# Kernel optimization log

Hardware: AMD Instinct MI355X
Metric: run time of the kernel (lower is better)

Reference implementation:

```python
import jax, jax.numpy as jnp
import numpy as np

N_NODES = 100000
N_EDGES = 1600000
N_GRAPHS = 256
D_IN = 128
D_HID = 128
D_OUT = 64


def graph_conv(x, src, dst, W_rel, b_rel, W_root):
    # PyG GraphConv: out = lin_rel(mean_{j->i} x_j) + lin_root(x)
    msgs = jax.ops.segment_sum(x[src], dst, num_segments=N_NODES)  # [N, d]
    deg = jax.ops.segment_sum(jnp.ones((src.shape[0],), x.dtype), dst, num_segments=N_NODES)
    agg = msgs / jnp.maximum(deg, 1.0)[:, None]
    return agg @ W_rel + b_rel + x @ W_root


def setup_inputs() -> dict:
    key = jax.random.key(0)
    ks = jax.random.split(key, 12)
    x = jax.random.normal(ks[0], (N_NODES, D_IN), dtype=jnp.float32)
    edge_index = jax.random.randint(ks[1], (2, N_EDGES), 0, N_NODES, dtype=jnp.int64)
    batch = jnp.sort(jax.random.randint(ks[2], (N_NODES,), 0, N_GRAPHS, dtype=jnp.int64))
    def lin(k, fan_in, fan_out):
        bound = 1.0 / np.sqrt(fan_in)
        return jax.random.uniform(k, (fan_in, fan_out), jnp.float32, -bound, bound)
    inp = {
        "x": x, "edge_index": edge_index, "batch": batch,
        "W1_rel": lin(ks[3], D_IN, D_HID), "b1_rel": jnp.zeros((D_HID,), jnp.float32), "W1_root": lin(ks[4], D_IN, D_HID),
        "W2_rel": lin(ks[5], D_HID, D_HID), "b2_rel": jnp.zeros((D_HID,), jnp.float32), "W2_root": lin(ks[6], D_HID, D_HID),
        "W3_rel": lin(ks[7], D_HID, D_HID), "b3_rel": jnp.zeros((D_HID,), jnp.float32), "W3_root": lin(ks[8], D_HID, D_HID),
        "Wl": lin(ks[9], D_HID, D_OUT), "bl": jnp.zeros((D_OUT,), jnp.float32),
    }
    return inp


def reference(x, edge_index, batch, W1_rel, b1_rel, W1_root, W2_rel, b2_rel, W2_root,
              W3_rel, b3_rel, W3_root, Wl, bl):
    src, dst = edge_index[0], edge_index[1]
    h = jax.nn.relu(graph_conv(x, src, dst, W1_rel, b1_rel, W1_root))
    h = jax.nn.relu(graph_conv(h, src, dst, W2_rel, b2_rel, W2_root))
    h = graph_conv(h, src, dst, W3_rel, b3_rel, W3_root)
    # global mean pool over graphs
    sums = jax.ops.segment_sum(h, batch, num_segments=N_GRAPHS)          # [G, d]
    cnts = jax.ops.segment_sum(jnp.ones((h.shape[0],), h.dtype), batch, num_segments=N_GRAPHS)
    pooled = sums / jnp.maximum(cnts, 1.0)[:, None]
    # dropout is identity at inference
    return pooled @ Wl + bl  # [G, D_OUT]
```

## Files before the change

### kernel.cpp

```cpp
#include <hip/hip_runtime.h>
#include <hip/hip_bf16.h>

#define N_NODES  100000
#define N_EDGES  1600000
#define N_GRAPHS 256
#define DCH      128
#define DOUT     64
#define NB       391
#define PADB     512
#define SLACK    4608
#define CHUNK    2048
#define PCH      32

typedef short v8s __attribute__((ext_vector_type(8)));
typedef float v4f __attribute__((ext_vector_type(4)));

static __device__ __forceinline__ float bf2f(unsigned short u) {
    unsigned int x = ((unsigned int)u) << 16;
    return __builtin_bit_cast(float, x);
}
static __device__ __forceinline__ unsigned short f2bf(float f) {
    unsigned int x = __builtin_bit_cast(unsigned int, f);
    unsigned int r = (x + 0x7fffu + ((x >> 16) & 1u)) >> 16;
    return (unsigned short)r;
}
static __device__ __forceinline__ int clampi(int v, int lo, int hi) {
    return v < lo ? lo : (v > hi ? hi : v);
}

__global__ void cvt_kernel(const float* __restrict__ in, unsigned short* __restrict__ out) {
    size_t i = ((size_t)blockIdx.x * blockDim.x + threadIdx.x) * 4;
    if (i + 3 < (size_t)N_NODES * DCH) {
        float4 f = *reinterpret_cast<const float4*>(in + i);
        uint2 o;
        o.x = ((unsigned)f2bf(f.y) << 16) | (unsigned)f2bf(f.x);
        o.y = ((unsigned)f2bf(f.w) << 16) | (unsigned)f2bf(f.z);
        *reinterpret_cast<uint2*>(out + i) = o;
    }
}

__global__ void __launch_bounds__(256) binA_kernel(const int* __restrict__ src, const int* __restrict__ dst,
                                                   int* __restrict__ gcur, uint2* __restrict__ region) {
    __shared__ uint2 stage[CHUNK];
    __shared__ int hcnt[PADB], hcnt2[PADB], hoff[PADB], garr[PADB];
    __shared__ int s2[256];
    int tid = threadIdx.x;
    int e0  = blockIdx.x * CHUNK;
    int nedge = N_EDGES - e0; if (nedge > CHUNK) nedge = CHUNK;

    for (int b = tid; b < PADB; b += 256) { hcnt[b] = 0; hcnt2[b] = 0; }
    __syncthreads();

    int es[CHUNK / 256], ed[CHUNK / 256];
    #pragma unroll
    for (int j = 0; j < CHUNK / 256; j++) {
        int e = e0 + j * 256 + tid;
        if (e < N_EDGES) {
            es[j] = clampi(src[e], 0, N_NODES - 1);
            ed[j] = clampi(dst[e], 0, N_NODES - 1);
            atomicAdd(&hcnt[ed[j] >> 8], 1);
        } else { es[j] = -1; ed[j] = 0; }
    }
    __syncthreads();

    int v0 = hcnt[2 * tid], v1 = hcnt[2 * tid + 1];
    s2[tid] = v0 + v1; __syncthreads();
    for (int off = 1; off < 256; off <<= 1) {
        int x = (tid >= off) ? s2[tid - off] : 0;
        __syncthreads();
        s2[tid] += x;
        __syncthreads();
    }
    int excl = s2[tid] - (v0 + v1);
    hoff[2 * tid] = excl; hoff[2 * tid + 1] = excl + v0;
    __syncthreads();

    for (int b = tid; b < NB; b += 256) {
        int c = hcnt[b];
        garr[b] = b * SLACK + ((c > 0) ? atomicAdd(&gcur[b], c) : 0);
    }
    __syncthreads();

    #pragma unroll
    for (int j = 0; j < CHUNK / 256; j++) {
        if (es[j] >= 0) {
            int b = ed[j] >> 8;
            int pos = atomicAdd(&hcnt2[b], 1) + hoff[b];
            stage[pos] = (uint2){(unsigned)es[j], (unsigned)ed[j]};
        }
    }
    __syncthreads();

    for (int i = tid; i < nedge; i += 256) {
        uint2 en = stage[i];
        int b = (int)(en.y >> 8);
        int gpos = garr[b] + (i - hoff[b]);
        if (gpos < (b + 1) * SLACK) region[gpos] = en;
    }
}

__global__ void __launch_bounds__(256) scan_kernel(const int* __restrict__ gcur,
                                                   int* __restrict__ hoffG, int* __restrict__ rowptr) {
    __shared__ int s2[256];
    int tid = threadIdx.x;
    int c0 = gcur[2 * tid];     if (c0 > SLACK) c0 = SLACK;
    int c1 = gcur[2 * tid + 1]; if (c1 > SLACK) c1 = SLACK;
    s2[tid] = c0 + c1; __syncthreads();
    for (int off = 1; off < 256; off <<= 1) {
        int x = (tid >= off) ? s2[tid - off] : 0;
        __syncthreads();
        s2[tid] += x;
        __syncthreads();
    }
    int excl = s2[tid] - (c0 + c1);
    hoffG[2 * tid] = excl; hoffG[2 * tid + 1] = excl + c0;
    if (tid == 255) rowptr[N_NODES] = s2[255];
}

__global__ void __launch_bounds__(256) binFinish_kernel(const uint2* __restrict__ region, const int* __restrict__ gcur,
                                                        const int* __restrict__ hoffG,
                                                        int* __restrict__ rowptr, int* __restrict__ csr) {
    __shared__ int h[256], sc[256], cur[256];
    int b = blockIdx.x, tid = threadIdx.x;
    h[tid] = 0;
    int base = hoffG[b];
    int size = gcur[b]; if (size > SLACK) size = SLACK;
    int node0 = b * 256;
    __syncthreads();
    for (int j = tid; j < size; j += 256) {
        unsigned loc = region[b * SLACK + j].y - (unsigned)node0;
        if (loc < 256u) atomicAdd(&h[loc], 1);
    }
    __syncthreads();
    int v = h[tid]; sc[tid] = v; __syncthreads();
    for (int off = 1; off < 256; off <<= 1) {
        int x = (tid >= off) ? sc[tid - off] : 0;
        __syncthreads();
        sc[tid] += x;
        __syncthreads();
    }
    int myptr = base + sc[tid] - v;
    int node = node0 + tid;
    if (node < N_NODES) rowptr[node] = myptr;
    cur[tid] = myptr;
    __syncthreads();
    for (int j = tid; j < size; j += 256) {
        uint2 en = region[b * SLACK + j];
        unsigned loc = en.y - (unsigned)node0;
        if (loc < 256u) {
            int p = atomicAdd(&cur[loc], 1);
            if (p >= 0 && p < N_EDGES) csr[p] = (int)en.x;
        }
    }
}

__global__ void wfrag_kernel(const float* __restrict__ W1rel, const float* __restrict__ W1root,
                             const float* __restrict__ W2rel, const float* __restrict__ W2root,
                             const float* __restrict__ W3rel, const float* __restrict__ W3root,
                             unsigned short* __restrict__ frag) {
    int gid = blockIdx.x * blockDim.x + threadIdx.x;
    if (gid >= 3 * 8 * 8 * 64) return;
    int lane = gid & 63;
    int nt   = (gid >> 6) & 7;
    int kt   = (gid >> 9) & 7;
    int L    = gid >> 12;
    const float* rel  = (L == 0) ? W1rel  : (L == 1) ? W2rel  : W3rel;
    const float* root = (L == 0) ? W1root : (L == 1) ? W2root : W3root;
    int n  = nt * 16 + (lane & 15);
    int k0 = kt * 32 + (lane >> 4) * 8;
    unsigned short o[8];
    #pragma unroll
    for (int j = 0; j < 8; j++) {
        int k = k0 + j;
        float w = (k < 128) ? rel[k * 128 + n] : root[(k - 128) * 128 + n];
        o[j] = f2bf(w);
    }
    uint4 u;
    u.x = (unsigned)o[0] | ((unsigned)o[1] << 16);
    u.y = (unsigned)o[2] | ((unsigned)o[3] << 16);
    u.z = (unsigned)o[4] | ((unsigned)o[5] << 16);
    u.w = (unsigned)o[6] | ((unsigned)o[7] << 16);
    *reinterpret_cast<uint4*>(frag + (size_t)gid * 8) = u;
}

__global__ void __launch_bounds__(128, 4) layer_kernel(
    const unsigned short* __restrict__ hin,
    const int* __restrict__ rowptr, const int* __restrict__ csr,
    const unsigned short* __restrict__ frag, const float* __restrict__ bias,
    unsigned short* __restrict__ hout, int relu)
{
    __shared__ __attribute__((aligned(16))) unsigned short As[2][32 * DCH];
    const int wave = threadIdx.x >> 6;
    const int lane = threadIdx.x & 63;
    const int l16  = lane & 15;
    const int quad = lane >> 4;
    const int base = blockIdx.x * 64 + wave * 32;
    if (base >= N_NODES) return;

    char* Asb = reinterpret_cast<char*>(As[wave]);

    int rp = rowptr[base + (lane < 33 ? lane : 32)];
    const int R0 = __builtin_amdgcn_readlane(rp, 0);
    const int R1 = __builtin_amdgcn_readlane(rp, 32);

    int ni     = 0;
    int nstart = R0;
    int nend   = __builtin_amdgcn_readlane(rp, 1);
    float a0 = 0.f, a1 = 0.f;

    int t0  = csr[R0 + l16];
    int idx = (R0 + l16 < R1) ? t0 : N_NODES;

    for (int e0 = R0; e0 < R1; e0 += 16) {
        int en   = e0 + 16 + l16;
        int tn   = csr[en];
        int idxn = (en < R1) ? tn : N_NODES;

        unsigned v[16];
        #pragma unroll
        for (int j = 0; j < 16; j++) {
            int s = __builtin_amdgcn_readlane(idx, j);
            v[j] = *reinterpret_cast<const unsigned*>(hin + (size_t)s * DCH + lane * 2);
        }

        #pragma unroll
        for (int j = 0; j < 16; j++) {
            int e = e0 + j;
            while (ni < 32 && e == nend) {
                int deg = nend - nstart;
                float inv = 1.0f / (float)(deg > 1 ? deg : 1);
                unsigned o = ((unsigned)f2bf(a1 * inv) << 16) | (unsigned)f2bf(a0 * inv);
                *reinterpret_cast<unsigned*>(Asb + ni * 256 + ((lane * 4) ^ ((ni & 7) << 4))) = o;
                a0 = 0.f; a1 = 0.f;
                ni++;
                nstart = nend;
                nend = __builtin_amdgcn_readlane(rp, ni + 1);
            }
            a0 += bf2f((unsigned short)(v[j] & 0xffffu));
            a1 += bf2f((unsigned short)(v[j] >> 16));
        }
        idx = idxn;
    }
    while (ni < 32) {
        int deg = nend - nstart;
        float inv = 1.0f / (float)(deg > 1 ? deg : 1);
        unsigned o = ((unsigned)f2bf(a1 * inv) << 16) | (unsigned)f2bf(a0 * inv);
        *reinterpret_cast<unsigned*>(Asb + ni * 256 + ((lane * 4) ^ ((ni & 7) << 4))) = o;
        a0 = 0.f; a1 = 0.f;
        ni++;
        nstart = nend;
        nend = __builtin_amdgcn_readlane(rp, ni + 1 < 33 ? ni + 1 : 32);
    }

    v4f acc[2][8];
    #pragma unroll
    for (int h = 0; h < 2; h++)
        #pragma unroll
        for (int nt = 0; nt < 8; nt++) acc[h][nt] = (v4f){0.f, 0.f, 0.f, 0.f};

    #pragma unroll
    for (int kt = 0; kt < 8; kt++) {
        v8s a0v, a1v;
        if (kt < 4) {
            int co = (kt * 64 + quad * 16) ^ ((l16 & 7) << 4);
            a0v = *reinterpret_cast<const v8s*>(Asb + l16 * 256 + co);
            a1v = *reinterpret_cast<const v8s*>(Asb + (16 + l16) * 256 + co);
        } else {
            int ak = (kt - 4) * 32 + quad * 8;
            a0v = *reinterpret_cast<const v8s*>(hin + (size_t)(base + l16) * DCH + ak);
            a1v = *reinterpret_cast<const v8s*>(hin + (size_t)(base + 16 + l16) * DCH + ak);
        }
        #pragma unroll
        for (int nt = 0; nt < 8; nt++) {
            v8s b = *reinterpret_cast<const v8s*>(frag + (((size_t)(kt * 8 + nt)) * 64 + lane) * 8);
            acc[0][nt] = __builtin_amdgcn_mfma_f32_16x16x32_bf16(a0v, b, acc[0][nt], 0, 0, 0);
            acc[1][nt] = __builtin_amdgcn_mfma_f32_16x16x32_bf16(a1v, b, acc[1][nt], 0, 0, 0);
        }
    }
    #pragma unroll
    for (int h = 0; h < 2; h++) {
        int mbase = base + h * 16 + quad * 4;
        #pragma unroll
        for (int nt = 0; nt < 8; nt++) {
            int n = nt * 16 + l16;
            float bv = bias[n];
            #pragma unroll
            for (int r = 0; r < 4; r++) {
                float v = acc[h][nt][r] + bv;
                if (relu) v = fmaxf(v, 0.f);
                hout[(size_t)(mbase + r) * DCH + n] = f2bf(v);
            }
        }
    }
}

__global__ void __launch_bounds__(128) pool_kernel(const unsigned short* __restrict__ h,
                                                   const int* __restrict__ batch,
                                                   float* __restrict__ psum) {
    int c  = threadIdx.x;
    int n0 = blockIdx.x * PCH;
    int n1 = n0 + PCH < N_NODES ? n0 + PCH : N_NODES;
    if (n0 >= n1) return;
    int cur = clampi(batch[n0], 0, N_GRAPHS - 1);
    float acc = 0.f;
    for (int n = n0; n < n1; n++) {
        int g = clampi(batch[n], 0, N_GRAPHS - 1);
        if (g != cur) {
            atomicAdd(&psum[cur * DCH + c], acc);
            acc = 0.f; cur = g;
        }
        acc += bf2f(h[(size_t)n * DCH + c]);
    }
    atomicAdd(&psum[cur * DCH + c], acc);
}

static __device__ __forceinline__ int lowerb(const int* __restrict__ a, int n, int key) {
    int lo = 0, hi = n;
    while (lo < hi) { int mid = (lo + hi) >> 1; if (a[mid] < key) lo = mid + 1; else hi = mid; }
    return lo;
}

__global__ void __launch_bounds__(64) final_kernel(const float* __restrict__ psum,
                                                   const int* __restrict__ batch,
                                                   const float* __restrict__ Wl, const float* __restrict__ bl,
                                                   float* __restrict__ out) {
    __shared__ float ps[DCH];
    __shared__ int bounds[2];
    int g = blockIdx.x, tid = threadIdx.x;
    if (tid == 0) {
        bounds[0] = lowerb(batch, N_NODES, g);
        bounds[1] = lowerb(batch, N_NODES, g + 1);
    }
    __syncthreads();
    int cnt = bounds[1] - bounds[0];
    float inv = 1.0f / (float)(cnt > 1 ? cnt : 1);
    ps[tid] = psum[g * DCH + tid] * inv;
    ps[tid + 64] = psum[g * DCH + tid + 64] * inv;
    __syncthreads();
    float o = 0.f;
    #pragma unroll 4
    for (int c = 0; c < DCH; c++) o += ps[c] * Wl[c * DOUT + tid];
    out[g * DOUT + tid] = o + bl[tid];
}

extern "C" void kernel_launch(void* const* d_in, const int* in_sizes, int n_in,
                              void* d_out, int out_size, void* d_ws, size_t ws_size,
                              hipStream_t stream) {
    const float* x     = (const float*)d_in[0];
    const int*   edge  = (const int*)d_in[1];
    const int*   src   = edge;
    const int*   dst   = edge + N_EDGES;
    const int*   batch = (const int*)d_in[2];
    const float* W1rel  = (const float*)d_in[3];
    const float* b1     = (const float*)d_in[4];
    const float* W1root = (const float*)d_in[5];
    const float* W2rel  = (const float*)d_in[6];
    const float* b2     = (const float*)d_in[7];
    const float* W2root = (const float*)d_in[8];
    const float* W3rel  = (const float*)d_in[9];
    const float* b3     = (const float*)d_in[10];
    const float* W3root = (const float*)d_in[11];
    const float* Wl     = (const float*)d_in[12];
    const float* bl     = (const float*)d_in[13];
    float* out = (float*)d_out;

    char* ws = (char*)d_ws;
    size_t off = 0;
    auto carve = [&](size_t bytes) -> void* {
        void* p = ws + off;
        off += (bytes + 255) & ~(size_t)255;
        return p;
    };
    int*            rowptr  = (int*)carve((size_t)(N_NODES + 1) * 4);
    int*            csr     = (int*)carve((size_t)(N_EDGES + 64) * 4);
    int*            gcur    = (int*)carve((size_t)PADB * 4 + (size_t)N_GRAPHS * DCH * 4);
    float*          psum    = (float*)(gcur + PADB);
    int*            hoffG   = (int*)carve((size_t)PADB * 4);
    unsigned short* frag    = (unsigned short*)carve((size_t)3 * 8 * 8 * 64 * 8 * 2);
    unsigned short* B1      = (unsigned short*)carve((size_t)(N_NODES + 1) * DCH * 2);
    unsigned short* B2      = (unsigned short*)carve((size_t)(N_NODES + 1) * DCH * 2);
    uint2*          region  = (uint2*)B1;

    hipMemsetAsync(gcur, 0, (size_t)PADB * 4 + (size_t)N_GRAPHS * DCH * 4, stream);
    hipMemsetAsync(B1 + (size_t)N_NODES * DCH, 0, (size_t)DCH * 2, stream);
    hipMemsetAsync(B2 + (size_t)N_NODES * DCH, 0, (size_t)DCH * 2, stream);

    binA_kernel<<<(N_EDGES + CHUNK - 1) / CHUNK, 256, 0, stream>>>(src, dst, gcur, region);
    scan_kernel<<<1, 256, 0, stream>>>(gcur, hoffG, rowptr);
    binFinish_kernel<<<NB, 256, 0, stream>>>(region, gcur, hoffG, rowptr, csr);
    cvt_kernel<<<(N_NODES * DCH / 4 + 255) / 256, 256, 0, stream>>>(x, B2);
    wfrag_kernel<<<(3 * 8 * 8 * 64 + 255) / 256, 256, 0, stream>>>(W1rel, W1root, W2rel, W2root, W3rel, W3root, frag);

    const int layerGrid = (N_NODES + 63) / 64;

    layer_kernel<<<layerGrid, 128, 0, stream>>>(B2, rowptr, csr, frag,         b1, B1, 1);
    layer_kernel<<<layerGrid, 128, 0, stream>>>(B1, rowptr, csr, frag + 32768, b2, B2, 1);
    layer_kernel<<<layerGrid, 128, 0, stream>>>(B2, rowptr, csr, frag + 65536, b3, B1, 0);

    pool_kernel<<<(N_NODES + PCH - 1) / PCH, 128, 0, stream>>>(B1, batch, psum);
    final_kernel<<<N_GRAPHS, 64, 0, stream>>>(psum, batch, Wl, bl, out);
}
```

Before: 414.9 us.

## Fuse mean-pool into last layer, merge prep kernels, use 16-row waves

The third GraphConv layer now accumulates its bias-added outputs straight into the per-graph pool sums with atomics, which removes the separate pool kernel and the write and re-read of the final hidden features. Input conversion, weight fragment packing and zeroing of the padding rows are merged into one prep kernel, replacing two launches and two memsets. The layer kernel now gives each wave 16 nodes instead of 32, with 256-thread blocks. This spreads the gather work over more waves for better latency hiding, at the cost of reusing each weight fragment across half as many rows.

```diff
diff --git a/kernel.cpp b/kernel.cpp
--- a/kernel.cpp
+++ b/kernel.cpp
@@ -10,7 +10,6 @@
 #define PADB     512
 #define SLACK    4608
 #define CHUNK    2048
-#define PCH      32
 
 typedef short v8s __attribute__((ext_vector_type(8)));
 typedef float v4f __attribute__((ext_vector_type(4)));
@@ -26,17 +25,6 @@
 }
 static __device__ __forceinline__ int clampi(int v, int lo, int hi) {
     return v < lo ? lo : (v > hi ? hi : v);
-}
-
-__global__ void cvt_kernel(const float* __restrict__ in, unsigned short* __restrict__ out) {
-    size_t i = ((size_t)blockIdx.x * blockDim.x + threadIdx.x) * 4;
-    if (i + 3 < (size_t)N_NODES * DCH) {
-        float4 f = *reinterpret_cast<const float4*>(in + i);
-        uint2 o;
-        o.x = ((unsigned)f2bf(f.y) << 16) | (unsigned)f2bf(f.x);
-        o.y = ((unsigned)f2bf(f.w) << 16) | (unsigned)f2bf(f.z);
-        *reinterpret_cast<uint2*>(out + i) = o;
-    }
 }
 
 __global__ void __launch_bounds__(256) binA_kernel(const int* __restrict__ src, const int* __restrict__ dst,
@@ -154,54 +142,71 @@
     }
 }
 
-__global__ void wfrag_kernel(const float* __restrict__ W1rel, const float* __restrict__ W1root,
-                             const float* __restrict__ W2rel, const float* __restrict__ W2root,
-                             const float* __restrict__ W3rel, const float* __restrict__ W3root,
-                             unsigned short* __restrict__ frag) {
-    int gid = blockIdx.x * blockDim.x + threadIdx.x;
-    if (gid >= 3 * 8 * 8 * 64) return;
-    int lane = gid & 63;
-    int nt   = (gid >> 6) & 7;
-    int kt   = (gid >> 9) & 7;
-    int L    = gid >> 12;
-    const float* rel  = (L == 0) ? W1rel  : (L == 1) ? W2rel  : W3rel;
-    const float* root = (L == 0) ? W1root : (L == 1) ? W2root : W3root;
-    int n  = nt * 16 + (lane & 15);
-    int k0 = kt * 32 + (lane >> 4) * 8;
-    unsigned short o[8];
-    #pragma unroll
-    for (int j = 0; j < 8; j++) {
-        int k = k0 + j;
-        float w = (k < 128) ? rel[k * 128 + n] : root[(k - 128) * 128 + n];
-        o[j] = f2bf(w);
-    }
-    uint4 u;
-    u.x = (unsigned)o[0] | ((unsigned)o[1] << 16);
-    u.y = (unsigned)o[2] | ((unsigned)o[3] << 16);
-    u.z = (unsigned)o[4] | ((unsigned)o[5] << 16);
-    u.w = (unsigned)o[6] | ((unsigned)o[7] << 16);
-    *reinterpret_cast<uint4*>(frag + (size_t)gid * 8) = u;
-}
-
-__global__ void __launch_bounds__(128, 4) layer_kernel(
+__global__ void __launch_bounds__(256) prep_kernel(const float* __restrict__ x, unsigned short* __restrict__ B2,
+                                                   const float* __restrict__ W1rel, const float* __restrict__ W1root,
+                                                   const float* __restrict__ W2rel, const float* __restrict__ W2root,
+                                                   const float* __restrict__ W3rel, const float* __restrict__ W3root,
+                                                   unsigned short* __restrict__ frag,
+                                                   unsigned short* __restrict__ z1, unsigned short* __restrict__ z2) {
+    int bid = blockIdx.x, tid = threadIdx.x;
+    if (bid < 12500) {
+        size_t i = ((size_t)bid * 256 + tid) * 4;
+        float4 f = *reinterpret_cast<const float4*>(x + i);
+        uint2 o;
+        o.x = ((unsigned)f2bf(f.y) << 16) | (unsigned)f2bf(f.x);
+        o.y = ((unsigned)f2bf(f.w) << 16) | (unsigned)f2bf(f.z);
+        *reinterpret_cast<uint2*>(B2 + i) = o;
+    } else if (bid < 12548) {
+        int gid = (bid - 12500) * 256 + tid;
+        int lane = gid & 63;
+        int nt   = (gid >> 6) & 7;
+        int kt   = (gid >> 9) & 7;
+        int L    = gid >> 12;
+        const float* rel  = (L == 0) ? W1rel  : (L == 1) ? W2rel  : W3rel;
+        const float* root = (L == 0) ? W1root : (L == 1) ? W2root : W3root;
+        int n  = nt * 16 + (lane & 15);
+        int k0 = kt * 32 + (lane >> 4) * 8;
+        unsigned short o[8];
+        #pragma unroll
+        for (int j = 0; j < 8; j++) {
+            int k = k0 + j;
+            float w = (k < 128) ? rel[k * 128 + n] : root[(k - 128) * 128 + n];
+            o[j] = f2bf(w);
+        }
+        uint4 u;
+        u.x = (unsigned)o[0] | ((unsigned)o[1] << 16);
+        u.y = (unsigned)o[2] | ((unsigned)o[3] << 16);
+        u.z = (unsigned)o[4] | ((unsigned)o[5] << 16);
+        u.w = (unsigned)o[6] | ((unsigned)o[7] << 16);
+        *reinterpret_cast<uint4*>(frag + (size_t)gid * 8) = u;
+    } else {
+        if (tid < 64)       reinterpret_cast<unsigned*>(z1)[tid] = 0;
+        else if (tid < 128) reinterpret_cast<unsigned*>(z2)[tid - 64] = 0;
+    }
+}
+
+__global__ void __launch_bounds__(256, 6) layer_kernel(
     const unsigned short* __restrict__ hin,
     const int* __restrict__ rowptr, const int* __restrict__ csr,
     const unsigned short* __restrict__ frag, const float* __restrict__ bias,
-    unsigned short* __restrict__ hout, int relu)
+    unsigned short* __restrict__ hout,
+    const int* __restrict__ batch, float* __restrict__ psum, int mode)
 {
-    __shared__ __attribute__((aligned(16))) unsigned short As[2][32 * DCH];
+    __shared__ __attribute__((aligned(16))) unsigned short As[4][16 * DCH];
     const int wave = threadIdx.x >> 6;
     const int lane = threadIdx.x & 63;
     const int l16  = lane & 15;
     const int quad = lane >> 4;
-    const int base = blockIdx.x * 64 + wave * 32;
+    const int base = blockIdx.x * 64 + wave * 16;
     if (base >= N_NODES) return;
 
     char* Asb = reinterpret_cast<char*>(As[wave]);
 
-    int rp = rowptr[base + (lane < 33 ? lane : 32)];
+    int ridx = base + (lane < 17 ? lane : 16);
+    if (ridx > N_NODES) ridx = N_NODES;
+    int rp = rowptr[ridx];
     const int R0 = __builtin_amdgcn_readlane(rp, 0);
-    const int R1 = __builtin_amdgcn_readlane(rp, 32);
+    const int R1 = __builtin_amdgcn_readlane(rp, 16);
 
     int ni     = 0;
     int nstart = R0;
@@ -226,7 +231,7 @@
         #pragma unroll
         for (int j = 0; j < 16; j++) {
             int e = e0 + j;
-            while (ni < 32 && e == nend) {
+            while (ni < 16 && e == nend) {
                 int deg = nend - nstart;
                 float inv = 1.0f / (float)(deg > 1 ? deg : 1);
                 unsigned o = ((unsigned)f2bf(a1 * inv) << 16) | (unsigned)f2bf(a0 * inv);
@@ -234,14 +239,14 @@
                 a0 = 0.f; a1 = 0.f;
                 ni++;
                 nstart = nend;
-                nend = __builtin_amdgcn_readlane(rp, ni + 1);
+                nend = __builtin_amdgcn_readlane(rp, ni + 1 < 17 ? ni + 1 : 16);
             }
             a0 += bf2f((unsigned short)(v[j] & 0xffffu));
             a1 += bf2f((unsigned short)(v[j] >> 16));
         }
         idx = idxn;
     }
-    while (ni < 32) {
+    while (ni < 16) {
         int deg = nend - nstart;
         float inv = 1.0f / (float)(deg > 1 ? deg : 1);
         unsigned o = ((unsigned)f2bf(a1 * inv) << 16) | (unsigned)f2bf(a0 * inv);
@@ -249,69 +254,84 @@
         a0 = 0.f; a1 = 0.f;
         ni++;
         nstart = nend;
-        nend = __builtin_amdgcn_readlane(rp, ni + 1 < 33 ? ni + 1 : 32);
-    }
-
-    v4f acc[2][8];
+        nend = __builtin_amdgcn_readlane(rp, ni + 1 < 17 ? ni + 1 : 16);
+    }
+
+    v4f acc[8];
     #pragma unroll
-    for (int h = 0; h < 2; h++)
-        #pragma unroll
-        for (int nt = 0; nt < 8; nt++) acc[h][nt] = (v4f){0.f, 0.f, 0.f, 0.f};
+    for (int nt = 0; nt < 8; nt++) acc[nt] = (v4f){0.f, 0.f, 0.f, 0.f};
 
     #pragma unroll
     for (int kt = 0; kt < 8; kt++) {
-        v8s a0v, a1v;
+        v8s av;
         if (kt < 4) {
             int co = (kt * 64 + quad * 16) ^ ((l16 & 7) << 4);
-            a0v = *reinterpret_cast<const v8s*>(Asb + l16 * 256 + co);
-            a1v = *reinterpret_cast<const v8s*>(Asb + (16 + l16) * 256 + co);
+            av = *reinterpret_cast<const v8s*>(Asb + l16 * 256 + co);
         } else {
             int ak = (kt - 4) * 32 + quad * 8;
-            a0v = *reinterpret_cast<const v8s*>(hin + (size_t)(base + l16) * DCH + ak);
-            a1v = *reinterpret_cast<const v8s*>(hin + (size_t)(base + 16 + l16) * DCH + ak);
+            int row = base + l16; if (row > N_NODES) row = N_NODES;
+            av = *reinterpret_cast<const v8s*>(hin + (size_t)row * DCH + ak);
         }
         #pragma unroll
         for (int nt = 0; nt < 8; nt++) {
             v8s b = *reinterpret_cast<const v8s*>(frag + (((size_t)(kt * 8 + nt)) * 64 + lane) * 8);
-            acc[0][nt] = __builtin_amdgcn_mfma_f32_16x16x32_bf16(a0v, b, acc[0][nt], 0, 0, 0);
-            acc[1][nt] = __builtin_amdgcn_mfma_f32_16x16x32_bf16(a1v, b, acc[1][nt], 0, 0, 0);
-        }
-    }
-    #pragma unroll
-    for (int h = 0; h < 2; h++) {
-        int mbase = base + h * 16 + quad * 4;
+            acc[nt] = __builtin_amdgcn_mfma_f32_16x16x32_bf16(av, b, acc[nt], 0, 0, 0);
+        }
+    }
+
+    if (mode != 2) {
         #pragma unroll
         for (int nt = 0; nt < 8; nt++) {
             int n = nt * 16 + l16;
             float bv = bias[n];
             #pragma unroll
             for (int r = 0; r < 4; r++) {
-                float v = acc[h][nt][r] + bv;
-                if (relu) v = fmaxf(v, 0.f);
-                hout[(size_t)(mbase + r) * DCH + n] = f2bf(v);
+                int row = base + quad * 4 + r;
+                if (row < N_NODES) {
+                    float v = acc[nt][r] + bv;
+                    if (mode == 1) v = fmaxf(v, 0.f);
+                    hout[(size_t)row * DCH + n] = f2bf(v);
+                }
             }
         }
-    }
-}
-
-__global__ void __launch_bounds__(128) pool_kernel(const unsigned short* __restrict__ h,
-                                                   const int* __restrict__ batch,
-                                                   float* __restrict__ psum) {
-    int c  = threadIdx.x;
-    int n0 = blockIdx.x * PCH;
-    int n1 = n0 + PCH < N_NODES ? n0 + PCH : N_NODES;
-    if (n0 >= n1) return;
-    int cur = clampi(batch[n0], 0, N_GRAPHS - 1);
-    float acc = 0.f;
-    for (int n = n0; n < n1; n++) {
-        int g = clampi(batch[n], 0, N_GRAPHS - 1);
-        if (g != cur) {
-            atomicAdd(&psum[cur * DCH + c], acc);
-            acc = 0.f; cur = g;
-        }
-        acc += bf2f(h[(size_t)n * DCH + c]);
-    }
-    atomicAdd(&psum[cur * DCH + c], acc);
+    } else {
+        int last = base + 15;
+        bool fast = (last < N_NODES) && (batch[base] == batch[last]);
+        if (fast) {
+            int g = batch[base];
+            #pragma unroll
+            for (int nt = 0; nt < 8; nt++) {
+                int n = nt * 16 + l16;
+                float s = acc[nt][0] + acc[nt][1] + acc[nt][2] + acc[nt][3] + 4.0f * bias[n];
+                s += __shfl_xor(s, 16);
+                s += __shfl_xor(s, 32);
+                if (quad == 0) atomicAdd(&psum[g * DCH + n], s);
+            }
+        } else {
+            int g[4];
+            #pragma unroll
+            for (int r = 0; r < 4; r++) {
+                int row = base + quad * 4 + r;
+                g[r] = (row < N_NODES) ? batch[row] : -1;
+            }
+            #pragma unroll
+            for (int nt = 0; nt < 8; nt++) {
+                int n = nt * 16 + l16;
+                float bv = bias[n];
+                float s = 0.f; int cg = -1;
+                #pragma unroll
+                for (int r = 0; r < 4; r++) {
+                    if (g[r] < 0) continue;
+                    if (g[r] != cg) {
+                        if (cg >= 0) atomicAdd(&psum[cg * DCH + n], s);
+                        s = 0.f; cg = g[r];
+                    }
+                    s += acc[nt][r] + bv;
+                }
+                if (cg >= 0) atomicAdd(&psum[cg * DCH + n], s);
+            }
+        }
+    }
 }
 
 static __device__ __forceinline__ int lowerb(const int* __restrict__ a, int n, int key) {
@@ -382,21 +402,18 @@
     uint2*          region  = (uint2*)B1;
 
     hipMemsetAsync(gcur, 0, (size_t)PADB * 4 + (size_t)N_GRAPHS * DCH * 4, stream);
-    hipMemsetAsync(B1 + (size_t)N_NODES * DCH, 0, (size_t)DCH * 2, stream);
-    hipMemsetAsync(B2 + (size_t)N_NODES * DCH, 0, (size_t)DCH * 2, stream);
 
     binA_kernel<<<(N_EDGES + CHUNK - 1) / CHUNK, 256, 0, stream>>>(src, dst, gcur, region);
     scan_kernel<<<1, 256, 0, stream>>>(gcur, hoffG, rowptr);
     binFinish_kernel<<<NB, 256, 0, stream>>>(region, gcur, hoffG, rowptr, csr);
-    cvt_kernel<<<(N_NODES * DCH / 4 + 255) / 256, 256, 0, stream>>>(x, B2);
-    wfrag_kernel<<<(3 * 8 * 8 * 64 + 255) / 256, 256, 0, stream>>>(W1rel, W1root, W2rel, W2root, W3rel, W3root, frag);
+    prep_kernel<<<12549, 256, 0, stream>>>(x, B2, W1rel, W1root, W2rel, W2root, W3rel, W3root,
+                                           frag, B1 + (size_t)N_NODES * DCH, B2 + (size_t)N_NODES * DCH);
 
     const int layerGrid = (N_NODES + 63) / 64;
 
-    layer_kernel<<<layerGrid, 128, 0, stream>>>(B2, rowptr, csr, frag,         b1, B1, 1);
-    layer_kernel<<<layerGrid, 128, 0, stream>>>(B1, rowptr, csr, frag + 32768, b2, B2, 1);
-    layer_kernel<<<layerGrid, 128, 0, stream>>>(B2, rowptr, csr, frag + 65536, b3, B1, 0);
-
-    pool_kernel<<<(N_NODES + PCH - 1) / PCH, 128, 0, stream>>>(B1, batch, psum);
+    layer_kernel<<<layerGrid, 256, 0, stream>>>(B2, rowptr, csr, frag,         b1, B1, batch, psum, 1);
+    layer_kernel<<<layerGrid, 256, 0, stream>>>(B1, rowptr, csr, frag + 32768, b2, B2, batch, psum, 1);
+    layer_kernel<<<layerGrid, 256, 0, stream>>>(B2, rowptr, csr, frag + 65536, b3, B1, batch, psum, 2);
+
     final_kernel<<<N_GRAPHS, 64, 0, stream>>>(psum, batch, Wl, bl, out);
 }
```

Result: no change. 411.4 us (-0.8%).
